# Kernel tuning notes

Hardware: AMD Instinct MI355X
Metric: run time of the kernel (lower is better)

Reference implementation:

```python
import jax, jax.numpy as jnp
import numpy as np

N = 20000   # nodes
E = 100000  # edges per relation
R = 4       # relations
H = 4       # heads
D = 64      # embed_dim (per-head dim == embed_dim in this module)
F = 128     # node_feat_dim
L = 2       # layers
EPS = 1e-5  # torch LayerNorm default


def setup_inputs() -> dict:
    key = jax.random.key(0)
    ks = jax.random.split(key, 32)
    s = 0.05
    inp = {}
    inp["nodes"] = jnp.arange(N)
    inp["node_features"] = jax.random.normal(ks[0], (N, F), jnp.float32)
    inp["betweenness"] = jax.random.uniform(ks[1], (N,), jnp.float32)
    inp["closeness"] = jax.random.uniform(ks[2], (N,), jnp.float32)
    inp["node_sign_influence"] = jax.random.normal(ks[3], (N,), jnp.float32)
    inp["edge_src"] = jax.random.randint(ks[4], (R, E), 0, N)
    inp["edge_tgt"] = jax.random.randint(ks[5], (R, E), 0, N)
    # encoder params
    inp["enc_Wf"] = jax.random.normal(ks[6], (F, D), jnp.float32) * s
    inp["enc_bf"] = jnp.full((D,), 0.01, jnp.float32)
    inp["enc_Wc"] = jax.random.normal(ks[7], (2, D), jnp.float32) * s
    inp["enc_bc"] = jnp.full((D,), 0.01, jnp.float32)
    # per-layer, per-relation attention params
    inp["Wq"] = jax.random.normal(ks[8], (L, R, D, D * H), jnp.float32) * s
    inp["bq"] = jnp.zeros((L, R, D * H), jnp.float32)
    inp["Wk"] = jax.random.normal(ks[9], (L, R, D, D * H), jnp.float32) * s
    inp["bk"] = jnp.zeros((L, R, D * H), jnp.float32)
    inp["Wv"] = jax.random.normal(ks[10], (L, R, D, D * H), jnp.float32) * s
    inp["bv"] = jnp.zeros((L, R, D * H), jnp.float32)
    inp["Wp"] = jax.random.normal(ks[11], (L, R * H * D, D), jnp.float32) * s
    inp["bp"] = jnp.zeros((L, D), jnp.float32)
    inp["sign_w"] = jax.random.normal(ks[12], (L, H, R), jnp.float32) * s
    inp["ln_g"] = jnp.ones((L, D), jnp.float32)
    inp["ln_b"] = jnp.zeros((L, D), jnp.float32)
    return inp


def reference(nodes, node_features, betweenness, closeness, node_sign_influence,
              edge_src, edge_tgt, enc_Wf, enc_bf, enc_Wc, enc_bc,
              Wq, bq, Wk, bk, Wv, bv, Wp, bp, sign_w, ln_g, ln_b):
    # CentralityAwareEncoder
    cen = jnp.stack([betweenness[nodes], closeness[nodes]], axis=1)  # [N, 2]
    x = node_features[nodes] @ enc_Wf + enc_bf + cen @ enc_Wc + enc_bc  # [N, D]
    n = x.shape[0]
    inv_sqrt_d = 1.0 / jnp.sqrt(jnp.float32(D))
    for l in range(L):  # structural loop over layers
        outs = []
        for r in range(R):  # structural loop over relations
            src, tgt = edge_src[r], edge_tgt[r]
            Q = (x @ Wq[l, r] + bq[l, r]).reshape(n, H, D)
            K = (x @ Wk[l, r] + bk[l, r]).reshape(n, H, D)
            V = (x @ Wv[l, r] + bv[l, r]).reshape(n, H, D)
            # edge-wise scores [E, H]
            scores = jnp.einsum('ehd,ehd->eh', Q[src], K[tgt]) * inv_sqrt_d
            scores = scores * (node_sign_influence[src][:, None] * sign_w[l, :, r][None, :])
            # segment softmax over src (all heads at once)
            mx = jax.ops.segment_max(scores, src, num_segments=n)
            ex = jnp.exp(scores - mx[src])
            den = jax.ops.segment_sum(ex, src, num_segments=n)
            attn = ex / (den[src] + 1e-10)  # [E, H]  (dropout: eval mode, identity)
            wV = V[tgt] * attn[..., None]   # [E, H, D]
            out = jax.ops.segment_sum(wV, src, num_segments=n)  # [N, H, D]
            outs.append(out.reshape(n, H * D))
        attn_out = jnp.concatenate(outs, axis=-1) @ Wp[l] + bp[l]  # [N, D]
        y = x + attn_out
        mu = y.mean(-1, keepdims=True)
        var = y.var(-1, keepdims=True)
        x = (y - mu) * jax.lax.rsqrt(var + EPS) * ln_g[l] + ln_b[l]
    return x
```

## Files before the change

kernel.cpp:

```cpp
#include <hip/hip_runtime.h>
#include <math.h>

#define NN 20000
#define EE 100000
#define RR 4
#define HH 4
#define DD 64
#define FF 128
#define LL 2
#define NB 79

typedef __attribute__((ext_vector_type(8))) short bf16x8;
typedef __attribute__((ext_vector_type(4))) float f32x4;

__device__ __forceinline__ ushort f2bf(float f) {
  uint u = __float_as_uint(f);
  u += 0x7FFFu + ((u >> 16) & 1u);
  return (ushort)(u >> 16);
}
__device__ __forceinline__ float bf2f(ushort h) {
  return __uint_as_float((uint)h << 16);
}

__global__ __launch_bounds__(256) void encoder_kernel(
    const float* __restrict__ feat, const float* __restrict__ bet,
    const float* __restrict__ clo, const float* __restrict__ Wf,
    const float* __restrict__ bf, const float* __restrict__ Wc,
    const float* __restrict__ bc, float* __restrict__ x,
    ushort* __restrict__ xbf) {
  __shared__ float fs[4][FF];
  const int t = threadIdx.x;
  const int n0 = blockIdx.x * 4;
  for (int idx = t; idx < 4 * FF; idx += 256) {
    const int rr = idx >> 7, cc = idx & 127;
    const int n = n0 + rr;
    fs[rr][cc] = (n < NN) ? feat[(size_t)n * FF + cc] : 0.f;
  }
  __syncthreads();
  const int g = t >> 6, d = t & 63;
  const int n = n0 + g;
  if (n >= NN) return;
  float acc = bf[d] + bc[d] + bet[n] * Wc[d] + clo[n] * Wc[DD + d];
#pragma unroll 8
  for (int f = 0; f < FF; ++f) acc = fmaf(fs[g][f], Wf[f * DD + d], acc);
  x[(size_t)n * DD + d] = acc;
  xbf[(size_t)n * DD + d] = f2bf(acc);
}

__global__ __launch_bounds__(256) void prep_kernel(
    const float* __restrict__ Wq, const float* __restrict__ bq,
    const float* __restrict__ Wk, const float* __restrict__ bk,
    const float* __restrict__ Wv, const float* __restrict__ bv,
    const float* __restrict__ Wp, ushort* __restrict__ mT,
    ushort* __restrict__ gT, float* __restrict__ cvec,
    float* __restrict__ gam) {
  const int idx = blockIdx.x * 256 + threadIdx.x;
  const int R1 = LL * RR * 272 * 64;
  const int R2 = LL * 64 * 1024;
  if (idx < R1) {
    const int lr = idx / (272 * 64);
    const int rem = idx % (272 * 64);
    const int col = rem >> 6, i = rem & 63;
    const float* wq = Wq + (size_t)lr * 64 * 256;
    const float* wk = Wk + (size_t)lr * 64 * 256;
    float v = 0.f;
    if (col < 256) {
      const int h = col >> 6, j = col & 63;
      const float* qa = wq + (size_t)i * 256 + h * 64;
      const float* kb = wk + (size_t)j * 256 + h * 64;
#pragma unroll 8
      for (int d = 0; d < 64; ++d) v = fmaf(qa[d], kb[d], v);
    } else if (col < 260) {
      const int h = col - 256;
      const float* qa = wq + (size_t)i * 256 + h * 64;
      const float* bb = bk + lr * 256 + h * 64;
#pragma unroll 8
      for (int d = 0; d < 64; ++d) v = fmaf(qa[d], bb[d], v);
    } else if (col < 264) {
      const int h = col - 260;
      const float* ka = wk + (size_t)i * 256 + h * 64;
      const float* bb = bq + lr * 256 + h * 64;
#pragma unroll 8
      for (int d = 0; d < 64; ++d) v = fmaf(ka[d], bb[d], v);
    }
    mT[idx] = f2bf(v);
  } else if (idx < R1 + R2) {
    const int id = idx - R1;
    const int lj = id >> 10;
    const int k = id & 1023;
    const int l = lj >> 6, j = lj & 63;
    const int r = k >> 8, h = (k >> 6) & 3, v_ = k & 63;
    const float* wv = Wv + (size_t)(l * RR + r) * 64 * 256 + (size_t)v_ * 256 + h * 64;
    const float* wp = Wp + (size_t)l * 65536 + (size_t)(r * 256 + h * 64) * 64 + j;
    float s = 0.f;
#pragma unroll 8
    for (int d = 0; d < 64; ++d) s = fmaf(wv[d], wp[d * 64], s);
    gT[id] = f2bf(s);
  } else if (idx < R1 + R2 + 512) {
    const int id = idx - R1 - R2;
    const int l = id >> 8, rj = id & 255;
    const int r = rj >> 6, j = rj & 63;
    const float* bb = bv + (l * RR + r) * 256;
    const float* wp = Wp + (size_t)l * 65536 + (size_t)(r * 256) * 64 + j;
    float s = 0.f;
    for (int q2 = 0; q2 < 256; ++q2) s = fmaf(bb[q2], wp[q2 * 64], s);
    cvec[id] = s;
  } else if (idx < R1 + R2 + 512 + 32) {
    const int id = idx - R1 - R2 - 512;
    const int lr = id >> 2, h = id & 3;
    const float* a = bq + lr * 256 + h * 64;
    const float* b2 = bk + lr * 256 + h * 64;
    float s = 0.f;
    for (int d = 0; d < 64; ++d) s = fmaf(a[d], b2[d], s);
    gam[id] = s;
  }
}

__global__ __launch_bounds__(256) void hist_kernel(
    const int* __restrict__ esrc, int* __restrict__ counts) {
  const int e = blockIdx.x * 256 + threadIdx.x;
  const int r = blockIdx.y;
  if (e < EE) atomicAdd(&counts[r * NN + esrc[(size_t)r * EE + e]], 1);
}

__global__ __launch_bounds__(256) void scanA_kernel(
    const int* __restrict__ counts, int* __restrict__ offs,
    int* __restrict__ bsum) {
  __shared__ int tmp[256];
  const int r = blockIdx.y, bx = blockIdx.x, t = threadIdx.x;
  const int i = bx * 256 + t;
  tmp[t] = (i < NN) ? counts[r * NN + i] : 0;
  __syncthreads();
#pragma unroll
  for (int s = 1; s < 256; s <<= 1) {
    const int add = (t >= s) ? tmp[t - s] : 0;
    __syncthreads();
    tmp[t] += add;
    __syncthreads();
  }
  if (i < NN) offs[r * (NN + 1) + i + 1] = tmp[t];
  if (t == 255) bsum[r * NB + bx] = tmp[255];
}

__global__ __launch_bounds__(128) void scanB_kernel(int* __restrict__ bsum) {
  __shared__ int tmp[128];
  const int r = blockIdx.x, t = threadIdx.x;
  tmp[t] = (t < NB) ? bsum[r * NB + t] : 0;
  __syncthreads();
#pragma unroll
  for (int s = 1; s < 128; s <<= 1) {
    const int add = (t >= s) ? tmp[t - s] : 0;
    __syncthreads();
    tmp[t] += add;
    __syncthreads();
  }
  if (t < NB) bsum[r * NB + t] = (t == 0) ? 0 : tmp[t - 1];
}

__global__ __launch_bounds__(256) void scanC_kernel(
    const int* __restrict__ bsum, int* __restrict__ offs) {
  const int r = blockIdx.y, bx = blockIdx.x, t = threadIdx.x;
  const int i = bx * 256 + t;
  if (i < NN) offs[r * (NN + 1) + i + 1] += bsum[r * NB + bx];
  if (i == 0) offs[r * (NN + 1)] = 0;
}

__global__ __launch_bounds__(256) void fill_kernel(
    const int* __restrict__ esrc, const int* __restrict__ etgt,
    const int* __restrict__ offs, int* __restrict__ cursor,
    int* __restrict__ csr) {
  const int e = blockIdx.x * 256 + threadIdx.x;
  const int r = blockIdx.y;
  if (e < EE) {
    const int s = esrc[(size_t)r * EE + e];
    const int pos = offs[r * (NN + 1) + s] + atomicAdd(&cursor[r * NN + s], 1);
    csr[(size_t)r * EE + pos] = etgt[(size_t)r * EE + e];
  }
}

__global__ __launch_bounds__(256) void ygemm_kernel(
    const ushort* __restrict__ xbf, const ushort* __restrict__ mT_l,
    ushort* __restrict__ Y, ushort* __restrict__ ab) {
  const int t = threadIdx.x;
  const int w = t >> 6, l = t & 63;
  const int hi = l >> 4, lo = l & 15;
  const int m0 = blockIdx.x * 64;
  const int r = blockIdx.y / 5;
  const int tile = blockIdx.y % 5;
  const ushort* wT = mT_l + (size_t)r * 17408;
  const int row = min(m0 + w * 16 + lo, NN - 1);
  const ushort* arow = xbf + (size_t)row * 64 + hi * 8;
  const bf16x8 a0 = *(const bf16x8*)(arow);
  const bf16x8 a1 = *(const bf16x8*)(arow + 32);
  if (tile < 4) {
    const int n0 = tile * 64;
    f32x4 acc[4];
#pragma unroll
    for (int nt = 0; nt < 4; ++nt) {
      const ushort* brow = wT + (size_t)(n0 + nt * 16 + lo) * 64 + hi * 8;
      const bf16x8 b0 = *(const bf16x8*)(brow);
      const bf16x8 b1 = *(const bf16x8*)(brow + 32);
      f32x4 z = {0.f, 0.f, 0.f, 0.f};
      z = __builtin_amdgcn_mfma_f32_16x16x32_bf16(a0, b0, z, 0, 0, 0);
      z = __builtin_amdgcn_mfma_f32_16x16x32_bf16(a1, b1, z, 0, 0, 0);
      acc[nt] = z;
    }
    __shared__ ushort cs[64][72];
#pragma unroll
    for (int nt = 0; nt < 4; ++nt) {
#pragma unroll
      for (int i = 0; i < 4; ++i) {
        cs[w * 16 + hi * 4 + i][nt * 16 + lo] = f2bf(acc[nt][i]);
      }
    }
    __syncthreads();
    const int rr = t >> 2, c0 = (t & 3) * 16;
    const int gm = m0 + rr;
    if (gm < NN) {
      const uint4 v0 = *(const uint4*)&cs[rr][c0];
      const uint4 v1 = *(const uint4*)&cs[rr][c0 + 8];
      ushort* dst = Y + ((size_t)r * NN + gm) * 256 + n0 + c0;
      *(uint4*)(dst) = v0;
      *(uint4*)(dst + 8) = v1;
    }
  } else {
    const ushort* brow = wT + (size_t)(256 + lo) * 64 + hi * 8;
    const bf16x8 b0 = *(const bf16x8*)(brow);
    const bf16x8 b1 = *(const bf16x8*)(brow + 32);
    f32x4 z = {0.f, 0.f, 0.f, 0.f};
    z = __builtin_amdgcn_mfma_f32_16x16x32_bf16(a0, b0, z, 0, 0, 0);
    z = __builtin_amdgcn_mfma_f32_16x16x32_bf16(a1, b1, z, 0, 0, 0);
#pragma unroll
    for (int i = 0; i < 4; ++i) {
      const int gm = m0 + w * 16 + hi * 4 + i;
      if (gm < NN && lo < 8) {
        ab[((size_t)r * NN + gm) * 8 + lo] = f2bf(z[i]);
      }
    }
  }
}

__global__ __launch_bounds__(256) void attn_kernel(
    const ushort* __restrict__ xbf, const ushort* __restrict__ Y,
    const ushort* __restrict__ ab, const int* __restrict__ offs4,
    const int* __restrict__ csr4, const float* __restrict__ nsi,
    const float* __restrict__ sw_l, const float* __restrict__ gam_l,
    ushort* __restrict__ attr) {
  const int n = blockIdx.x;
  const int t = threadIdx.x;
  const int r = t >> 6, l = t & 63;
  const int h = l >> 4, lo = l & 15;
  const int* offs = offs4 + r * (NN + 1);
  const int* csr = csr4 + (size_t)r * EE;
  const ushort4 yu = *(const ushort4*)(Y + ((size_t)r * NN + n) * 256 + l * 4);
  const float y0 = bf2f(yu.x), y1 = bf2f(yu.y), y2 = bf2f(yu.z),
              y3 = bf2f(yu.w);
  const float c2 = 0.18033688f * nsi[n] * sw_l[h * RR + r];
  const float ac2 =
      (bf2f(ab[((size_t)r * NN + n) * 8 + h]) + gam_l[r * 4 + h]) * c2;
  const int s0 = offs[n], e0 = offs[n + 1];
  float den = 0.f;
  float o0 = 0.f, o1 = 0.f, o2 = 0.f, o3 = 0.f;
  if (s0 < e0) {
    int tg = __builtin_amdgcn_readfirstlane(csr[s0]);
    ushort4 xu = *(const ushort4*)(xbf + (size_t)tg * 64 + lo * 4);
    ushort beu = ab[((size_t)r * NN + tg) * 8 + 4 + h];
    for (int i = s0; i < e0; ++i) {
      const ushort4 cx = xu;
      const ushort cb = beu;
      if (i + 1 < e0) {
        tg = __builtin_amdgcn_readfirstlane(csr[i + 1]);
        xu = *(const ushort4*)(xbf + (size_t)tg * 64 + lo * 4);
        beu = ab[((size_t)r * NN + tg) * 8 + 4 + h];
      }
      const float x0 = bf2f(cx.x), x1 = bf2f(cx.y), x2 = bf2f(cx.z),
                  x3 = bf2f(cx.w);
      float d = y0 * x0;
      d = fmaf(y1, x1, d);
      d = fmaf(y2, x2, d);
      d = fmaf(y3, x3, d);
#pragma unroll
      for (int dd = 1; dd < 16; dd <<= 1) d += __shfl_xor(d, dd);
      const float pre = fmaf(bf2f(cb), c2, ac2);
      const float sc = fmaf(d, c2, pre);
      const float ew = __builtin_amdgcn_exp2f(sc);
      den += ew;
      o0 = fmaf(ew, x0, o0);
      o1 = fmaf(ew, x1, o1);
      o2 = fmaf(ew, x2, o2);
      o3 = fmaf(ew, x3, o3);
    }
  }
  const float inv = 1.f / (den + 1e-10f);
  ushort4 ou;
  ou.x = f2bf(o0 * inv);
  ou.y = f2bf(o1 * inv);
  ou.z = f2bf(o2 * inv);
  ou.w = f2bf(o3 * inv);
  *(ushort4*)(attr + (size_t)n * 1024 + r * 256 + l * 4) = ou;
}

__global__ __launch_bounds__(256) void proj_ln_kernel(
    const ushort* __restrict__ attr, const ushort* __restrict__ gT,
    const float* __restrict__ xin, const float* __restrict__ bp,
    const float* __restrict__ g, const float* __restrict__ b,
    const int* __restrict__ offs4, const float* __restrict__ cvec_l,
    float* __restrict__ xout, ushort* __restrict__ xbf_out) {
  __shared__ float red[4][64][20];
  const int t = threadIdx.x;
  const int w = t >> 6, l = t & 63;
  const int hi = l >> 4, lo = l & 15;
  const int m0 = blockIdx.x * 16;
  const ushort* arow = attr + (size_t)(m0 + lo) * 1024 + w * 256 + hi * 8;
  f32x4 acc[4] = {{0.f, 0.f, 0.f, 0.f},
                  {0.f, 0.f, 0.f, 0.f},
                  {0.f, 0.f, 0.f, 0.f},
                  {0.f, 0.f, 0.f, 0.f}};
#pragma unroll
  for (int ks = 0; ks < 8; ++ks) {
    const bf16x8 a = *(const bf16x8*)(arow + ks * 32);
#pragma unroll
    for (int nt = 0; nt < 4; ++nt) {
      const bf16x8 bb = *(const bf16x8*)(gT + (size_t)(nt * 16 + lo) * 1024 +
                                         w * 256 + ks * 32 + hi * 8);
      acc[nt] = __builtin_amdgcn_mfma_f32_16x16x32_bf16(a, bb, acc[nt], 0, 0, 0);
    }
  }
#pragma unroll
  for (int nt = 0; nt < 4; ++nt) *(f32x4*)&red[w][l][nt * 4] = acc[nt];
  __syncthreads();
  if (w == 0) {
    f32x4 fin[4];
#pragma unroll
    for (int nt = 0; nt < 4; ++nt) {
      f32x4 s = *(const f32x4*)&red[0][l][nt * 4];
      s += *(const f32x4*)&red[1][l][nt * 4];
      s += *(const f32x4*)&red[2][l][nt * 4];
      s += *(const f32x4*)&red[3][l][nt * 4];
      fin[nt] = s;
    }
#pragma unroll
    for (int i = 0; i < 4; ++i) {
      const int gr = m0 + hi * 4 + i;
      float fl[4];
#pragma unroll
      for (int r = 0; r < 4; ++r) {
        fl[r] = (offs4[r * (NN + 1) + gr + 1] > offs4[r * (NN + 1) + gr])
                    ? 1.f
                    : 0.f;
      }
      float y[4];
      float s = 0.f, s2 = 0.f;
#pragma unroll
      for (int nt = 0; nt < 4; ++nt) {
        const int col = nt * 16 + lo;
        float extra = fl[0] * cvec_l[col] + fl[1] * cvec_l[64 + col] +
                      fl[2] * cvec_l[128 + col] + fl[3] * cvec_l[192 + col];
        const float yv =
            fin[nt][i] + bp[col] + extra + xin[(size_t)gr * 64 + col];
        y[nt] = yv;
        s += yv;
        s2 = fmaf(yv, yv, s2);
      }
#pragma unroll
      for (int d = 1; d < 16; d <<= 1) {
        s += __shfl_xor(s, d);
        s2 += __shfl_xor(s2, d);
      }
      const float mu = s * (1.f / 64.f);
      const float var = s2 * (1.f / 64.f) - mu * mu;
      const float rstd = rsqrtf(var + 1e-5f);
#pragma unroll
      for (int nt = 0; nt < 4; ++nt) {
        const int col = nt * 16 + lo;
        const float xo = (y[nt] - mu) * rstd * g[col] + b[col];
        xout[(size_t)gr * 64 + col] = xo;
        if (xbf_out) xbf_out[(size_t)gr * 64 + col] = f2bf(xo);
      }
    }
  }
}

extern "C" void kernel_launch(void* const* d_in, const int* in_sizes, int n_in,
                              void* d_out, int out_size, void* d_ws,
                              size_t ws_size, hipStream_t stream) {
  const float* feat = (const float*)d_in[1];
  const float* bet = (const float*)d_in[2];
  const float* clo = (const float*)d_in[3];
  const float* nsi = (const float*)d_in[4];
  const int* esrc = (const int*)d_in[5];
  const int* etgt = (const int*)d_in[6];
  const float* Wf = (const float*)d_in[7];
  const float* bf = (const float*)d_in[8];
  const float* Wc = (const float*)d_in[9];
  const float* bc = (const float*)d_in[10];
  const float* Wq = (const float*)d_in[11];
  const float* bq = (const float*)d_in[12];
  const float* Wk = (const float*)d_in[13];
  const float* bk = (const float*)d_in[14];
  const float* Wv = (const float*)d_in[15];
  const float* bv = (const float*)d_in[16];
  const float* Wp = (const float*)d_in[17];
  const float* bp = (const float*)d_in[18];
  const float* sw = (const float*)d_in[19];
  const float* lng = (const float*)d_in[20];
  const float* lnb = (const float*)d_in[21];
  float* out = (float*)d_out;

  char* base = (char*)d_ws;
  size_t off = 0;
  auto alloc = [&](size_t bytes) {
    void* p = base + off;
    off += (bytes + 255) & ~(size_t)255;
    return p;
  };
  float* xa = (float*)alloc((size_t)NN * DD * 4);
  float* xb = (float*)alloc((size_t)NN * DD * 4);
  ushort* xbf = (ushort*)alloc((size_t)NN * DD * 2);
  ushort* Yb = (ushort*)alloc((size_t)RR * NN * 256 * 2);
  ushort* ab = (ushort*)alloc((size_t)RR * NN * 8 * 2);
  ushort* attr = (ushort*)alloc((size_t)NN * 1024 * 2);
  ushort* mT = (ushort*)alloc((size_t)LL * RR * 272 * 64 * 2);
  ushort* gT = (ushort*)alloc((size_t)LL * 64 * 1024 * 2);
  float* cvec = (float*)alloc((size_t)LL * RR * 64 * 4);
  float* gam = (float*)alloc((size_t)LL * RR * HH * 4);
  int* counts = (int*)alloc((size_t)RR * NN * 4);
  int* offsb = (int*)alloc((size_t)RR * (NN + 1) * 4);
  int* bsum = (int*)alloc((size_t)RR * NB * 4);
  int* csr = (int*)alloc((size_t)RR * EE * 4);
  (void)ws_size;

  hipMemsetAsync(counts, 0, (size_t)RR * NN * 4, stream);
  {
    dim3 gg((EE + 255) / 256, RR);
    hipLaunchKernelGGL(hist_kernel, gg, dim3(256), 0, stream, esrc, counts);
  }
  {
    dim3 gg(NB, RR);
    hipLaunchKernelGGL(scanA_kernel, gg, dim3(256), 0, stream, counts, offsb,
                       bsum);
    hipLaunchKernelGGL(scanB_kernel, dim3(RR), dim3(128), 0, stream, bsum);
    hipLaunchKernelGGL(scanC_kernel, gg, dim3(256), 0, stream, bsum, offsb);
  }
  hipMemsetAsync(counts, 0, (size_t)RR * NN * 4, stream);
  {
    dim3 gg((EE + 255) / 256, RR);
    hipLaunchKernelGGL(fill_kernel, gg, dim3(256), 0, stream, esrc, etgt, offsb,
                       counts, csr);
  }

  hipLaunchKernelGGL(prep_kernel, dim3(1059), dim3(256), 0, stream, Wq, bq, Wk,
                     bk, Wv, bv, Wp, mT, gT, cvec, gam);
  hipLaunchKernelGGL(encoder_kernel, dim3((NN + 3) / 4), dim3(256), 0, stream,
                     feat, bet, clo, Wf, bf, Wc, bc, xa, xbf);

  const int gm = (NN + 63) / 64;
  for (int l = 0; l < LL; ++l) {
    const float* xin = (l == 0) ? xa : xb;
    float* xout = (l == LL - 1) ? out : xb;
    ushort* xbf_next = (l == LL - 1) ? (ushort*)nullptr : xbf;
    hipLaunchKernelGGL(ygemm_kernel, dim3(gm, 20), dim3(256), 0, stream, xbf,
                       mT + (size_t)l * RR * 17408, Yb, ab);
    hipLaunchKernelGGL(attn_kernel, dim3(NN), dim3(256), 0, stream, xbf, Yb,
                       ab, offsb, csr, nsi, sw + l * HH * RR, gam + l * 16,
                       attr);
    hipLaunchKernelGGL(proj_ln_kernel, dim3(NN / 16), dim3(256), 0, stream,
                       attr, gT + (size_t)l * 65536, xin, bp + l * 64,
                       lng + l * 64, lnb + l * 64, offsb, cvec + l * 256, xout,
                       xbf_next);
  }
}
```

Baseline: 328.0 us.

## Merge scan kernels, fuse encoder with prep, and dual-accumulate attention loop

Replaces the three-kernel CSR offset scan with a single 1024-thread block per relation, and merges the encoder and weight-prep kernels into one launch split by block index. Together these cut the number of kernel launches. The attention edge loop now processes two edges per iteration with separate accumulators instead of software prefetching, exposing more independent loads and exp work. The single-block scan is serial-heavy per relation, and pairing the edges raises register use.

```diff
diff --git a/kernel.cpp b/kernel.cpp
--- a/kernel.cpp
+++ b/kernel.cpp
@@ -8,7 +8,6 @@
 #define DD 64
 #define FF 128
 #define LL 2
-#define NB 79
 
 typedef __attribute__((ext_vector_type(8))) short bf16x8;
 typedef __attribute__((ext_vector_type(4))) float f32x4;
@@ -22,39 +21,38 @@
   return __uint_as_float((uint)h << 16);
 }
 
-__global__ __launch_bounds__(256) void encoder_kernel(
+__global__ __launch_bounds__(256) void enc_prep_kernel(
     const float* __restrict__ feat, const float* __restrict__ bet,
     const float* __restrict__ clo, const float* __restrict__ Wf,
     const float* __restrict__ bf, const float* __restrict__ Wc,
     const float* __restrict__ bc, float* __restrict__ x,
-    ushort* __restrict__ xbf) {
-  __shared__ float fs[4][FF];
+    ushort* __restrict__ xbf, const float* __restrict__ Wq,
+    const float* __restrict__ bq, const float* __restrict__ Wk,
+    const float* __restrict__ bk, const float* __restrict__ Wv,
+    const float* __restrict__ bv, const float* __restrict__ Wp,
+    ushort* __restrict__ mT, ushort* __restrict__ gT, float* __restrict__ cvec,
+    float* __restrict__ gam) {
   const int t = threadIdx.x;
-  const int n0 = blockIdx.x * 4;
-  for (int idx = t; idx < 4 * FF; idx += 256) {
-    const int rr = idx >> 7, cc = idx & 127;
-    const int n = n0 + rr;
-    fs[rr][cc] = (n < NN) ? feat[(size_t)n * FF + cc] : 0.f;
-  }
-  __syncthreads();
-  const int g = t >> 6, d = t & 63;
-  const int n = n0 + g;
-  if (n >= NN) return;
-  float acc = bf[d] + bc[d] + bet[n] * Wc[d] + clo[n] * Wc[DD + d];
+  if (blockIdx.x < 5000) {
+    __shared__ float fs[4][FF];
+    const int n0 = blockIdx.x * 4;
+    for (int idx = t; idx < 4 * FF; idx += 256) {
+      const int rr = idx >> 7, cc = idx & 127;
+      const int n = n0 + rr;
+      fs[rr][cc] = (n < NN) ? feat[(size_t)n * FF + cc] : 0.f;
+    }
+    __syncthreads();
+    const int g = t >> 6, d = t & 63;
+    const int n = n0 + g;
+    if (n >= NN) return;
+    float acc = bf[d] + bc[d] + bet[n] * Wc[d] + clo[n] * Wc[DD + d];
 #pragma unroll 8
-  for (int f = 0; f < FF; ++f) acc = fmaf(fs[g][f], Wf[f * DD + d], acc);
-  x[(size_t)n * DD + d] = acc;
-  xbf[(size_t)n * DD + d] = f2bf(acc);
-}
-
-__global__ __launch_bounds__(256) void prep_kernel(
-    const float* __restrict__ Wq, const float* __restrict__ bq,
-    const float* __restrict__ Wk, const float* __restrict__ bk,
-    const float* __restrict__ Wv, const float* __restrict__ bv,
-    const float* __restrict__ Wp, ushort* __restrict__ mT,
-    ushort* __restrict__ gT, float* __restrict__ cvec,
-    float* __restrict__ gam) {
-  const int idx = blockIdx.x * 256 + threadIdx.x;
+    for (int f = 0; f < FF; ++f) acc = fmaf(fs[g][f], Wf[f * DD + d], acc);
+    x[(size_t)n * DD + d] = acc;
+    xbf[(size_t)n * DD + d] = f2bf(acc);
+    return;
+  }
+  const int idx = (blockIdx.x - 5000) * 256 + t;
   const int R1 = LL * RR * 272 * 64;
   const int R2 = LL * 64 * 1024;
   if (idx < R1) {
@@ -90,8 +88,10 @@
     const int k = id & 1023;
     const int l = lj >> 6, j = lj & 63;
     const int r = k >> 8, h = (k >> 6) & 3, v_ = k & 63;
-    const float* wv = Wv + (size_t)(l * RR + r) * 64 * 256 + (size_t)v_ * 256 + h * 64;
-    const float* wp = Wp + (size_t)l * 65536 + (size_t)(r * 256 + h * 64) * 64 + j;
+    const float* wv =
+        Wv + (size_t)(l * RR + r) * 64 * 256 + (size_t)v_ * 256 + h * 64;
+    const float* wp =
+        Wp + (size_t)l * 65536 + (size_t)(r * 256 + h * 64) * 64 + j;
     float s = 0.f;
 #pragma unroll 8
     for (int d = 0; d < 64; ++d) s = fmaf(wv[d], wp[d * 64], s);
@@ -123,46 +123,36 @@
   if (e < EE) atomicAdd(&counts[r * NN + esrc[(size_t)r * EE + e]], 1);
 }
 
-__global__ __launch_bounds__(256) void scanA_kernel(
-    const int* __restrict__ counts, int* __restrict__ offs,
-    int* __restrict__ bsum) {
-  __shared__ int tmp[256];
-  const int r = blockIdx.y, bx = blockIdx.x, t = threadIdx.x;
-  const int i = bx * 256 + t;
-  tmp[t] = (i < NN) ? counts[r * NN + i] : 0;
+__global__ __launch_bounds__(1024) void scan_kernel(
+    const int* __restrict__ counts, int* __restrict__ offs) {
+  __shared__ int ts[1024];
+  const int r = blockIdx.x, t = threadIdx.x;
+  const int base = t * 20;
+  int loc[20];
+  int run = 0;
+#pragma unroll
+  for (int k = 0; k < 20; ++k) {
+    const int i = base + k;
+    const int v = (i < NN) ? counts[r * NN + i] : 0;
+    run += v;
+    loc[k] = run;
+  }
+  ts[t] = run;
   __syncthreads();
 #pragma unroll
-  for (int s = 1; s < 256; s <<= 1) {
-    const int add = (t >= s) ? tmp[t - s] : 0;
+  for (int s = 1; s < 1024; s <<= 1) {
+    const int add = (t >= s) ? ts[t - s] : 0;
     __syncthreads();
-    tmp[t] += add;
+    ts[t] += add;
     __syncthreads();
   }
-  if (i < NN) offs[r * (NN + 1) + i + 1] = tmp[t];
-  if (t == 255) bsum[r * NB + bx] = tmp[255];
-}
-
-__global__ __launch_bounds__(128) void scanB_kernel(int* __restrict__ bsum) {
-  __shared__ int tmp[128];
-  const int r = blockIdx.x, t = threadIdx.x;
-  tmp[t] = (t < NB) ? bsum[r * NB + t] : 0;
-  __syncthreads();
-#pragma unroll
-  for (int s = 1; s < 128; s <<= 1) {
-    const int add = (t >= s) ? tmp[t - s] : 0;
-    __syncthreads();
-    tmp[t] += add;
-    __syncthreads();
-  }
-  if (t < NB) bsum[r * NB + t] = (t == 0) ? 0 : tmp[t - 1];
-}
-
-__global__ __launch_bounds__(256) void scanC_kernel(
-    const int* __restrict__ bsum, int* __restrict__ offs) {
-  const int r = blockIdx.y, bx = blockIdx.x, t = threadIdx.x;
-  const int i = bx * 256 + t;
-  if (i < NN) offs[r * (NN + 1) + i + 1] += bsum[r * NB + bx];
-  if (i == 0) offs[r * (NN + 1)] = 0;
+  const int prev = (t == 0) ? 0 : ts[t - 1];
+#pragma unroll
+  for (int k = 0; k < 20; ++k) {
+    const int i = base + k;
+    if (i < NN) offs[r * (NN + 1) + i + 1] = prev + loc[k];
+  }
+  if (t == 0) offs[r * (NN + 1)] = 0;
 }
 
 __global__ __launch_bounds__(256) void fill_kernel(
@@ -259,44 +249,74 @@
   const float ac2 =
       (bf2f(ab[((size_t)r * NN + n) * 8 + h]) + gam_l[r * 4 + h]) * c2;
   const int s0 = offs[n], e0 = offs[n + 1];
-  float den = 0.f;
-  float o0 = 0.f, o1 = 0.f, o2 = 0.f, o3 = 0.f;
-  if (s0 < e0) {
-    int tg = __builtin_amdgcn_readfirstlane(csr[s0]);
-    ushort4 xu = *(const ushort4*)(xbf + (size_t)tg * 64 + lo * 4);
-    ushort beu = ab[((size_t)r * NN + tg) * 8 + 4 + h];
-    for (int i = s0; i < e0; ++i) {
-      const ushort4 cx = xu;
-      const ushort cb = beu;
-      if (i + 1 < e0) {
-        tg = __builtin_amdgcn_readfirstlane(csr[i + 1]);
-        xu = *(const ushort4*)(xbf + (size_t)tg * 64 + lo * 4);
-        beu = ab[((size_t)r * NN + tg) * 8 + 4 + h];
-      }
-      const float x0 = bf2f(cx.x), x1 = bf2f(cx.y), x2 = bf2f(cx.z),
-                  x3 = bf2f(cx.w);
-      float d = y0 * x0;
-      d = fmaf(y1, x1, d);
-      d = fmaf(y2, x2, d);
-      d = fmaf(y3, x3, d);
-#pragma unroll
-      for (int dd = 1; dd < 16; dd <<= 1) d += __shfl_xor(d, dd);
-      const float pre = fmaf(bf2f(cb), c2, ac2);
-      const float sc = fmaf(d, c2, pre);
-      const float ew = __builtin_amdgcn_exp2f(sc);
-      den += ew;
-      o0 = fmaf(ew, x0, o0);
-      o1 = fmaf(ew, x1, o1);
-      o2 = fmaf(ew, x2, o2);
-      o3 = fmaf(ew, x3, o3);
-    }
-  }
-  const float inv = 1.f / (den + 1e-10f);
+  float denA = 0.f, oA0 = 0.f, oA1 = 0.f, oA2 = 0.f, oA3 = 0.f;
+  float denB = 0.f, oB0 = 0.f, oB1 = 0.f, oB2 = 0.f, oB3 = 0.f;
+  int i = s0;
+  for (; i + 1 < e0; i += 2) {
+    const int tgA = __builtin_amdgcn_readfirstlane(csr[i]);
+    const int tgB = __builtin_amdgcn_readfirstlane(csr[i + 1]);
+    const ushort4 cxA = *(const ushort4*)(xbf + (size_t)tgA * 64 + lo * 4);
+    const ushort4 cxB = *(const ushort4*)(xbf + (size_t)tgB * 64 + lo * 4);
+    const float bA = bf2f(ab[((size_t)r * NN + tgA) * 8 + 4 + h]);
+    const float bB = bf2f(ab[((size_t)r * NN + tgB) * 8 + 4 + h]);
+    const float xA0 = bf2f(cxA.x), xA1 = bf2f(cxA.y), xA2 = bf2f(cxA.z),
+                xA3 = bf2f(cxA.w);
+    const float xB0 = bf2f(cxB.x), xB1 = bf2f(cxB.y), xB2 = bf2f(cxB.z),
+                xB3 = bf2f(cxB.w);
+    float dA = y0 * xA0;
+    float dB = y0 * xB0;
+    dA = fmaf(y1, xA1, dA);
+    dB = fmaf(y1, xB1, dB);
+    dA = fmaf(y2, xA2, dA);
+    dB = fmaf(y2, xB2, dB);
+    dA = fmaf(y3, xA3, dA);
+    dB = fmaf(y3, xB3, dB);
+#pragma unroll
+    for (int dd = 1; dd < 16; dd <<= 1) {
+      dA += __shfl_xor(dA, dd);
+      dB += __shfl_xor(dB, dd);
+    }
+    const float scA = fmaf(dA, c2, fmaf(bA, c2, ac2));
+    const float scB = fmaf(dB, c2, fmaf(bB, c2, ac2));
+    const float ewA = __builtin_amdgcn_exp2f(scA);
+    const float ewB = __builtin_amdgcn_exp2f(scB);
+    denA += ewA;
+    denB += ewB;
+    oA0 = fmaf(ewA, xA0, oA0);
+    oB0 = fmaf(ewB, xB0, oB0);
+    oA1 = fmaf(ewA, xA1, oA1);
+    oB1 = fmaf(ewB, xB1, oB1);
+    oA2 = fmaf(ewA, xA2, oA2);
+    oB2 = fmaf(ewB, xB2, oB2);
+    oA3 = fmaf(ewA, xA3, oA3);
+    oB3 = fmaf(ewB, xB3, oB3);
+  }
+  if (i < e0) {
+    const int tg = __builtin_amdgcn_readfirstlane(csr[i]);
+    const ushort4 cx = *(const ushort4*)(xbf + (size_t)tg * 64 + lo * 4);
+    const float bb = bf2f(ab[((size_t)r * NN + tg) * 8 + 4 + h]);
+    const float x0 = bf2f(cx.x), x1 = bf2f(cx.y), x2 = bf2f(cx.z),
+                x3 = bf2f(cx.w);
+    float d = y0 * x0;
+    d = fmaf(y1, x1, d);
+    d = fmaf(y2, x2, d);
+    d = fmaf(y3, x3, d);
+#pragma unroll
+    for (int dd = 1; dd < 16; dd <<= 1) d += __shfl_xor(d, dd);
+    const float sc = fmaf(d, c2, fmaf(bb, c2, ac2));
+    const float ew = __builtin_amdgcn_exp2f(sc);
+    denA += ew;
+    oA0 = fmaf(ew, x0, oA0);
+    oA1 = fmaf(ew, x1, oA1);
+    oA2 = fmaf(ew, x2, oA2);
+    oA3 = fmaf(ew, x3, oA3);
+  }
+  const float inv = 1.f / (denA + denB + 1e-10f);
   ushort4 ou;
-  ou.x = f2bf(o0 * inv);
-  ou.y = f2bf(o1 * inv);
-  ou.z = f2bf(o2 * inv);
-  ou.w = f2bf(o3 * inv);
+  ou.x = f2bf((oA0 + oB0) * inv);
+  ou.y = f2bf((oA1 + oB1) * inv);
+  ou.z = f2bf((oA2 + oB2) * inv);
+  ou.w = f2bf((oA3 + oB3) * inv);
   *(ushort4*)(attr + (size_t)n * 1024 + r * 256 + l * 4) = ou;
 }
 
@@ -426,7 +446,6 @@
   float* gam = (float*)alloc((size_t)LL * RR * HH * 4);
   int* counts = (int*)alloc((size_t)RR * NN * 4);
   int* offsb = (int*)alloc((size_t)RR * (NN + 1) * 4);
-  int* bsum = (int*)alloc((size_t)RR * NB * 4);
   int* csr = (int*)alloc((size_t)RR * EE * 4);
   (void)ws_size;
 
@@ -435,13 +454,8 @@
     dim3 gg((EE + 255) / 256, RR);
     hipLaunchKernelGGL(hist_kernel, gg, dim3(256), 0, stream, esrc, counts);
   }
-  {
-    dim3 gg(NB, RR);
-    hipLaunchKernelGGL(scanA_kernel, gg, dim3(256), 0, stream, counts, offsb,
-                       bsum);
-    hipLaunchKernelGGL(scanB_kernel, dim3(RR), dim3(128), 0, stream, bsum);
-    hipLaunchKernelGGL(scanC_kernel, gg, dim3(256), 0, stream, bsum, offsb);
-  }
+  hipLaunchKernelGGL(scan_kernel, dim3(RR), dim3(1024), 0, stream, counts,
+                     offsb);
   hipMemsetAsync(counts, 0, (size_t)RR * NN * 4, stream);
   {
     dim3 gg((EE + 255) / 256, RR);
@@ -449,10 +463,9 @@
                        counts, csr);
   }
 
-  hipLaunchKernelGGL(prep_kernel, dim3(1059), dim3(256), 0, stream, Wq, bq, Wk,
-                     bk, Wv, bv, Wp, mT, gT, cvec, gam);
-  hipLaunchKernelGGL(encoder_kernel, dim3((NN + 3) / 4), dim3(256), 0, stream,
-                     feat, bet, clo, Wf, bf, Wc, bc, xa, xbf);
+  hipLaunchKernelGGL(enc_prep_kernel, dim3(6059), dim3(256), 0, stream, feat,
+                     bet, clo, Wf, bf, Wc, bc, xa, xbf, Wq, bq, Wk, bk, Wv, bv,
+                     Wp, mT, gT, cvec, gam);
 
   const int gm = (NN + 63) / 64;
   for (int l = 0; l < LL; ++l) {
```

Measured after the change: 314.6 us. 4.1% less time.
